# Performance work log

Hardware: AMD Instinct MI355X
Metric: run time of the kernel (lower is better)

Reference implementation:

```python
import jax, jax.numpy as jnp
import numpy as np

B, N, D, H = 4, 2048, 1024, 16
HD = D // H

def setup_inputs() -> dict:
    key = jax.random.key(0)
    ks = jax.random.split(key, 5)
    s = 0.02
    return {
        "x": jax.random.normal(ks[0], (B, N, D), dtype=jnp.float32),
        "W_qkv": jax.random.normal(ks[1], (D, 3 * D), dtype=jnp.float32) * s,
        "b_qkv": jnp.zeros((3 * D,), dtype=jnp.float32),
        "W_proj": jax.random.normal(ks[2], (D, D), dtype=jnp.float32) * s,
        "b_proj": jnp.zeros((D,), dtype=jnp.float32),
    }

def reference(x, W_qkv, b_qkv, W_proj, b_proj):
    scale = HD ** -0.5
    qkv = x @ W_qkv + b_qkv                       # [B,N,3D]
    qkv = qkv.reshape(B, N, 3, H, HD).transpose(2, 0, 3, 1, 4)  # [3,B,H,N,hd]
    q, k, v = qkv[0], qkv[1], qkv[2]
    attn = jnp.einsum('bhqd,bhkd->bhqk', q, k) * scale
    attn = jax.nn.softmax(attn, axis=-1)
    out = jnp.einsum('bhqk,bhkd->bhqd', attn, v)  # [B,H,N,hd]
    out = out.transpose(0, 2, 1, 3).reshape(B, N, D)
    return out @ W_proj + b_proj
```

## Files before the change

kernel.cpp:

```cpp
#include <hip/hip_runtime.h>


typedef __bf16 bf8v  __attribute__((ext_vector_type(8)));
typedef __bf16 bf4v  __attribute__((ext_vector_type(4)));
typedef float  f32x4 __attribute__((ext_vector_type(4)));

typedef const __attribute__((address_space(1))) void* gptr_t;
typedef __attribute__((address_space(3))) void*       lptr_t;

#define GLL16(g, l) __builtin_amdgcn_global_load_lds((gptr_t)(g), (lptr_t)(l), 16, 0, 0)

#define MFMA_BF16_16x16x32 __builtin_amdgcn_mfma_f32_16x16x32_bf16

static constexpr int Bsz = 4, Nseq = 2048, Dmod = 1024, H = 16, HD = 64;
static constexpr int Mtok = Bsz * Nseq;

__global__ __launch_bounds__(256) void cast_f32_bf16(const float* __restrict__ in,
                                                     __bf16* __restrict__ out, int n4) {
    int i = blockIdx.x * blockDim.x + threadIdx.x;
    int stride = gridDim.x * blockDim.x;
    for (; i < n4; i += stride) {
        float4 f = reinterpret_cast<const float4*>(in)[i];
        bf4v o;
        o[0] = (__bf16)f.x; o[1] = (__bf16)f.y; o[2] = (__bf16)f.z; o[3] = (__bf16)f.w;
        reinterpret_cast<bf4v*>(out)[i] = o;
    }
}

__global__ __launch_bounds__(256) void transpose_cast(const float* __restrict__ W,
                                                      __bf16* __restrict__ WT,
                                                      int K, int N) {
    __shared__ float t[32][33];
    int tx = threadIdx.x, ty = threadIdx.y;
    int bx = blockIdx.x, by = blockIdx.y;
#pragma unroll
    for (int j = 0; j < 4; ++j) {
        int k = by * 32 + ty + j * 8;
        int n = bx * 32 + tx;
        t[ty + j * 8][tx] = W[(size_t)k * N + n];
    }
    __syncthreads();
#pragma unroll
    for (int j = 0; j < 4; ++j) {
        int n = bx * 32 + ty + j * 8;
        int k = by * 32 + tx;
        WT[(size_t)n * K + k] = (__bf16)t[tx][ty + j * 8];
    }
}

__global__ __launch_bounds__(256) void transpose_v(const __bf16* __restrict__ V,
                                                   __bf16* __restrict__ VT) {
    __shared__ __bf16 Ls[64 * 72];
    const int t = threadIdx.x;
    const int blk = blockIdx.x;
    const int nt0 = (blk & 31) * 64;
    const size_t base = (size_t)(blk >> 5) * Nseq * HD;
#pragma unroll
    for (int i = 0; i < 2; ++i) {
        int c = i * 256 + t;
        int nt = c >> 3, p = c & 7;
        bf8v v8 = *(const bf8v*)&V[base + (size_t)(nt0 + nt) * HD + p * 8];
#pragma unroll
        for (int j = 0; j < 8; ++j)
            Ls[(p * 8 + j) * 72 + (nt ^ (p << 3))] = v8[j];
    }
    __syncthreads();
#pragma unroll
    for (int i = 0; i < 2; ++i) {
        int c = i * 256 + t;
        int hd = c >> 3, seg = c & 7;
        int key = (hd >> 3) << 3;
        bf8v o = *(const bf8v*)&Ls[hd * 72 + seg * 8];
        int ntb = (seg * 8) ^ (key << 3);
        ntb = (seg * 8) ^ ((hd >> 3) << 3);
        *(bf8v*)&VT[base + (size_t)hd * Nseq + nt0 + ntb] = o;
    }
}

template <int EPI>
__global__ __launch_bounds__(256) void gemm_bt(const __bf16* __restrict__ A,
                                               const __bf16* __restrict__ Bt,
                                               const float* __restrict__ bias,
                                               float* __restrict__ Cf,
                                               __bf16* __restrict__ Qo,
                                               __bf16* __restrict__ Ko,
                                               __bf16* __restrict__ Vo,
                                               int M, int N, int K) {
    __shared__ __attribute__((aligned(16))) __bf16 As[128 * 64];
    __shared__ __attribute__((aligned(16))) __bf16 Bs[128 * 64];

    const int nwg = gridDim.x;
    const int wg = (blockIdx.x & 7) * (nwg >> 3) + (blockIdx.x >> 3);

    const int nbn = N >> 7;
    const int bm = wg / nbn, bn = wg % nbn;
    const int tid = threadIdx.x;
    const int w = tid >> 6, l = tid & 63;
    const int wr = w >> 1, wc = w & 1;

    const int fr = l & 15;
    const int fk = (l >> 4) * 8;

    f32x4 acc[4][4] = {};

    for (int k0 = 0; k0 < K; k0 += 64) {
#pragma unroll
        for (int i = 0; i < 4; ++i) {
            int c = i * 256 + tid;
            int row = c >> 3, col = (c & 7) * 8;
            int scol = col ^ ((row & 7) << 3);
            GLL16(A + (size_t)(bm * 128 + row) * K + k0 + scol, &As[(i * 256 + w * 64) * 8]);
        }
#pragma unroll
        for (int i = 0; i < 4; ++i) {
            int c = i * 256 + tid;
            int row = c >> 3, col = (c & 7) * 8;
            int scol = col ^ ((row & 7) << 3);
            GLL16(Bt + (size_t)(bn * 128 + row) * K + k0 + scol, &Bs[(i * 256 + w * 64) * 8]);
        }
        __syncthreads();

#pragma unroll
        for (int kk = 0; kk < 2; ++kk) {
            bf8v af[4], bf[4];
#pragma unroll
            for (int m = 0; m < 4; ++m) {
                int row = wr * 64 + m * 16 + fr;
                af[m] = *(const bf8v*)&As[row * 64 + ((kk * 32 + fk) ^ ((row & 7) << 3))];
            }
#pragma unroll
            for (int n = 0; n < 4; ++n) {
                int row = wc * 64 + n * 16 + fr;
                bf[n] = *(const bf8v*)&Bs[row * 64 + ((kk * 32 + fk) ^ ((row & 7) << 3))];
            }
#pragma unroll
            for (int m = 0; m < 4; ++m)
#pragma unroll
                for (int n = 0; n < 4; ++n)
                    acc[m][n] = MFMA_BF16_16x16x32(af[m], bf[n], acc[m][n], 0, 0, 0);
        }
        __syncthreads();
    }

    const int r0 = bm * 128 + wr * 64;
    const int c0 = bn * 128 + wc * 64;
#pragma unroll
    for (int m = 0; m < 4; ++m)
#pragma unroll
        for (int n = 0; n < 4; ++n)
#pragma unroll
            for (int r = 0; r < 4; ++r) {
                int row = r0 + m * 16 + (l >> 4) * 4 + r;
                int col = c0 + n * 16 + (l & 15);
                float v = acc[m][n][r] + bias[col];
                if (EPI == 0) {
                    int mat = col >> 10, rem = col & 1023;
                    int h = rem >> 6, hd = rem & 63;
                    int b = row >> 11, nt = row & 2047;
                    size_t dst = (((size_t)(b * H + h)) * Nseq + nt) * HD + hd;
                    __bf16 val = (__bf16)v;
                    if (mat == 0)      Qo[dst] = val;
                    else if (mat == 1) Ko[dst] = val;
                    else               Vo[dst] = val;
                } else {
                    Cf[(size_t)row * N + col] = v;
                }
            }
}

__global__ __launch_bounds__(256, 3) void attn_kernel(const __bf16* __restrict__ Q,
                                                      const __bf16* __restrict__ K,
                                                      const __bf16* __restrict__ VT,
                                                      __bf16* __restrict__ Ao) {
    __shared__ __attribute__((aligned(16))) __bf16 Ks[2][64 * 64];
    __shared__ __attribute__((aligned(16))) __bf16 Vts[2][64 * 64];
    __shared__ __attribute__((aligned(16))) __bf16 Pl[4][32 * 72];

    const int tid = threadIdx.x;
    const int w = tid >> 6, l = tid & 63;

    const int nwg = gridDim.x;
    const int id = (blockIdx.x & 7) * (nwg >> 3) + (blockIdx.x >> 3);
    const int qb = id & 15;
    const int h = (id >> 4) & 15;
    const int b = id >> 8;
    const size_t base = (size_t)(b * H + h) * Nseq * HD;

    const int fr = l & 15;
    const int fkh = (l >> 4) * 8;

    const int sr0 = tid >> 3, sp0 = tid & 7;
    const int sr1 = (256 + tid) >> 3, sp1 = tid & 7;

    bf8v qf[2][2];
#pragma unroll
    for (int m = 0; m < 2; ++m) {
        const int qrow = qb * 128 + w * 32 + m * 16 + fr;
        qf[m][0] = *(const bf8v*)&Q[base + (size_t)qrow * HD + fkh];
        qf[m][1] = *(const bf8v*)&Q[base + (size_t)qrow * HD + 32 + fkh];
#pragma unroll
        for (int j = 0; j < 8; ++j) {
            qf[m][0][j] = (__bf16)((float)qf[m][0][j] * 0.125f);
            qf[m][1][j] = (__bf16)((float)qf[m][1][j] * 0.125f);
        }
    }

    f32x4 o[2][4] = {};
    f32x4 psum[2] = {};

#define STAGE(buf, kt)                                                                   \
    do {                                                                                 \
        GLL16(K  + base + (size_t)((kt) * 64 + sr0) * HD + ((sp0 ^ (sr0 & 7)) << 3),     \
              &Ks[buf][(w * 64) * 8]);                                                   \
        GLL16(K  + base + (size_t)((kt) * 64 + sr1) * HD + ((sp1 ^ (sr1 & 7)) << 3),     \
              &Ks[buf][(256 + w * 64) * 8]);                                             \
        GLL16(VT + base + (size_t)sr0 * Nseq + (kt) * 64 + ((sp0 ^ (sr0 & 7)) << 3),     \
              &Vts[buf][(w * 64) * 8]);                                                  \
        GLL16(VT + base + (size_t)sr1 * Nseq + (kt) * 64 + ((sp1 ^ (sr1 & 7)) << 3),     \
              &Vts[buf][(256 + w * 64) * 8]);                                            \
    } while (0)

    STAGE(0, 0);

    for (int kt = 0; kt < Nseq / 64; ++kt) {
        const int cur = kt & 1;
        if (kt < Nseq / 64 - 1) {
            STAGE(cur ^ 1, kt + 1);
            asm volatile("s_waitcnt vmcnt(4)" ::: "memory");
        } else {
            asm volatile("s_waitcnt vmcnt(0)" ::: "memory");
        }
        __builtin_amdgcn_s_barrier();

        f32x4 s[2][4];
        __builtin_amdgcn_s_setprio(1);
#pragma unroll
        for (int st = 0; st < 4; ++st) {
            const int krow = st * 16 + fr;
            const int key = (fr & 7) << 3;
            bf8v kf0 = *(const bf8v*)&Ks[cur][krow * 64 + (fkh ^ key)];
            bf8v kf1 = *(const bf8v*)&Ks[cur][krow * 64 + ((fkh + 32) ^ key)];
#pragma unroll
            for (int m = 0; m < 2; ++m) {
                f32x4 a = {};
                a = MFMA_BF16_16x16x32(qf[m][0], kf0, a, 0, 0, 0);
                a = MFMA_BF16_16x16x32(qf[m][1], kf1, a, 0, 0, 0);
                s[m][st] = a;
            }
        }
        __builtin_amdgcn_s_setprio(0);

#pragma unroll
        for (int m = 0; m < 2; ++m)
#pragma unroll
            for (int st = 0; st < 4; ++st)
#pragma unroll
                for (int r = 0; r < 4; ++r) {
                    float p = __expf(s[m][st][r]);
                    psum[m][r] += p;
                    const int qr = m * 16 + (l >> 4) * 4 + r;
                    Pl[w][qr * 72 + st * 16 + (l & 15)] = (__bf16)p;
                }

        bf8v pa[2][2];
#pragma unroll
        for (int m = 0; m < 2; ++m) {
            const int prow = m * 16 + fr;
            pa[m][0] = *(const bf8v*)&Pl[w][prow * 72 + fkh];
            pa[m][1] = *(const bf8v*)&Pl[w][prow * 72 + 32 + fkh];
        }
        __builtin_amdgcn_s_setprio(1);
#pragma unroll
        for (int t = 0; t < 4; ++t) {
            const int drow = t * 16 + fr;
            const int key = (fr & 7) << 3;
            bf8v vf0 = *(const bf8v*)&Vts[cur][drow * 64 + (fkh ^ key)];
            bf8v vf1 = *(const bf8v*)&Vts[cur][drow * 64 + ((fkh + 32) ^ key)];
#pragma unroll
            for (int m = 0; m < 2; ++m) {
                o[m][t] = MFMA_BF16_16x16x32(pa[m][0], vf0, o[m][t], 0, 0, 0);
                o[m][t] = MFMA_BF16_16x16x32(pa[m][1], vf1, o[m][t], 0, 0, 0);
            }
        }
        __builtin_amdgcn_s_setprio(0);
        __builtin_amdgcn_s_barrier();
    }
#undef STAGE

#pragma unroll
    for (int m = 0; m < 2; ++m)
#pragma unroll
        for (int r = 0; r < 4; ++r) {
            float ps = psum[m][r];
#pragma unroll
            for (int off = 1; off < 16; off <<= 1) ps += __shfl_xor(ps, off);
            psum[m][r] = 1.f / ps;
        }
#pragma unroll
    for (int m = 0; m < 2; ++m)
#pragma unroll
        for (int t = 0; t < 4; ++t)
#pragma unroll
            for (int r = 0; r < 4; ++r) {
                const int row = m * 16 + (l >> 4) * 4 + r;
                const int nq = qb * 128 + w * 32 + row;
                const int hd = t * 16 + (l & 15);
                Ao[((size_t)(b * Nseq + nq)) * Dmod + h * HD + hd] =
                    (__bf16)(o[m][t][r] * psum[m][r]);
            }
}

extern "C" void kernel_launch(void* const* d_in, const int* in_sizes, int n_in,
                              void* d_out, int out_size, void* d_ws, size_t ws_size,
                              hipStream_t stream) {
    const float* x      = (const float*)d_in[0];
    const float* W_qkv  = (const float*)d_in[1];
    const float* b_qkv  = (const float*)d_in[2];
    const float* W_proj = (const float*)d_in[3];
    const float* b_proj = (const float*)d_in[4];
    float* out = (float*)d_out;

    char* ws = (char*)d_ws;
    __bf16* Xb     = (__bf16*)(ws);
    __bf16* VTb    = (__bf16*)(ws);
    __bf16* WqkvT  = (__bf16*)(ws + 16777216);
    __bf16* WprojT = (__bf16*)(ws + 23068672);
    __bf16* Qb     = (__bf16*)(ws + 25165824);
    __bf16* Kb     = (__bf16*)(ws + 41943040);
    __bf16* Vb     = (__bf16*)(ws + 58720256);
    __bf16* Ab     = (__bf16*)(ws + 58720256);

    cast_f32_bf16<<<2048, 256, 0, stream>>>(x, Xb, Mtok * Dmod / 4);

    dim3 tb(32, 8);
    transpose_cast<<<dim3(3 * Dmod / 32, Dmod / 32), tb, 0, stream>>>(W_qkv, WqkvT, Dmod, 3 * Dmod);
    transpose_cast<<<dim3(Dmod / 32, Dmod / 32), tb, 0, stream>>>(W_proj, WprojT, Dmod, Dmod);

    gemm_bt<0><<<(Mtok / 128) * (3 * Dmod / 128), 256, 0, stream>>>(
        Xb, WqkvT, b_qkv, nullptr, Qb, Kb, Vb, Mtok, 3 * Dmod, Dmod);

    transpose_v<<<Bsz * H * (Nseq / 64), 256, 0, stream>>>(Vb, VTb);

    attn_kernel<<<Bsz * H * (Nseq / 128), 256, 0, stream>>>(Qb, Kb, VTb, Ab);

    gemm_bt<1><<<(Mtok / 128) * (Dmod / 128), 256, 0, stream>>>(
        Ab, WprojT, b_proj, out, nullptr, nullptr, nullptr, Mtok, Dmod, Dmod);
}
```

Before: 299.8 us.

## Switch attention to 32x32 MFMA with register-resident P via permlane swap

Rewrites the attention inner loop to use 32x32x16 MFMAs with S computed transposed (K as A operand), so the exponentiated probabilities stay in registers. The P tile is repacked with v_cvt_pk_bf16_f32 and v_permlane32_swap into the A-operand layout for the PV MFMA, which removes the per-wave LDS round trip for P and the Pl shared buffer. Row sums reduce with one cross-half shuffle, and the epilogue is rewritten for the 32x32 output layout. This cuts LDS traffic and LDS capacity, but it depends on getting the lane-mapping transpose exactly right, and the output stores are now strided per row.

```diff
diff --git a/kernel.cpp b/kernel.cpp
--- a/kernel.cpp
+++ b/kernel.cpp
@@ -1,9 +1,10 @@
 #include <hip/hip_runtime.h>
 
 
-typedef __bf16 bf8v  __attribute__((ext_vector_type(8)));
-typedef __bf16 bf4v  __attribute__((ext_vector_type(4)));
-typedef float  f32x4 __attribute__((ext_vector_type(4)));
+typedef __bf16 bf8v   __attribute__((ext_vector_type(8)));
+typedef __bf16 bf4v   __attribute__((ext_vector_type(4)));
+typedef float  f32x4  __attribute__((ext_vector_type(4)));
+typedef float  f32x16 __attribute__((ext_vector_type(16)));
 
 typedef const __attribute__((address_space(1))) void* gptr_t;
 typedef __attribute__((address_space(3))) void*       lptr_t;
@@ -11,6 +12,7 @@
 #define GLL16(g, l) __builtin_amdgcn_global_load_lds((gptr_t)(g), (lptr_t)(l), 16, 0, 0)
 
 #define MFMA_BF16_16x16x32 __builtin_amdgcn_mfma_f32_16x16x32_bf16
+#define MFMA_BF16_32x32x16 __builtin_amdgcn_mfma_f32_32x32x16_bf16
 
 static constexpr int Bsz = 4, Nseq = 2048, Dmod = 1024, H = 16, HD = 64;
 static constexpr int Mtok = Bsz * Nseq;
@@ -69,10 +71,8 @@
     for (int i = 0; i < 2; ++i) {
         int c = i * 256 + t;
         int hd = c >> 3, seg = c & 7;
-        int key = (hd >> 3) << 3;
         bf8v o = *(const bf8v*)&Ls[hd * 72 + seg * 8];
-        int ntb = (seg * 8) ^ (key << 3);
-        ntb = (seg * 8) ^ ((hd >> 3) << 3);
+        int ntb = (seg * 8) ^ ((hd >> 3) << 3);
         *(bf8v*)&VT[base + (size_t)hd * Nseq + nt0 + ntb] = o;
     }
 }
@@ -174,10 +174,11 @@
                                                       __bf16* __restrict__ Ao) {
     __shared__ __attribute__((aligned(16))) __bf16 Ks[2][64 * 64];
     __shared__ __attribute__((aligned(16))) __bf16 Vts[2][64 * 64];
-    __shared__ __attribute__((aligned(16))) __bf16 Pl[4][32 * 72];
 
     const int tid = threadIdx.x;
     const int w = tid >> 6, l = tid & 63;
+    const int lq = l & 31;
+    const int hi = l >> 5;
 
     const int nwg = gridDim.x;
     const int id = (blockIdx.x & 7) * (nwg >> 3) + (blockIdx.x >> 3);
@@ -186,27 +187,21 @@
     const int b = id >> 8;
     const size_t base = (size_t)(b * H + h) * Nseq * HD;
 
-    const int fr = l & 15;
-    const int fkh = (l >> 4) * 8;
-
     const int sr0 = tid >> 3, sp0 = tid & 7;
     const int sr1 = (256 + tid) >> 3, sp1 = tid & 7;
 
-    bf8v qf[2][2];
-#pragma unroll
-    for (int m = 0; m < 2; ++m) {
-        const int qrow = qb * 128 + w * 32 + m * 16 + fr;
-        qf[m][0] = *(const bf8v*)&Q[base + (size_t)qrow * HD + fkh];
-        qf[m][1] = *(const bf8v*)&Q[base + (size_t)qrow * HD + 32 + fkh];
-#pragma unroll
-        for (int j = 0; j < 8; ++j) {
-            qf[m][0][j] = (__bf16)((float)qf[m][0][j] * 0.125f);
-            qf[m][1][j] = (__bf16)((float)qf[m][1][j] * 0.125f);
-        }
-    }
-
-    f32x4 o[2][4] = {};
-    f32x4 psum[2] = {};
+    const int qrow = qb * 128 + w * 32 + lq;
+    bf8v qf[4];
+#pragma unroll
+    for (int c = 0; c < 4; ++c) {
+        qf[c] = *(const bf8v*)&Q[base + (size_t)qrow * HD + c * 16 + hi * 8];
+#pragma unroll
+        for (int j = 0; j < 8; ++j)
+            qf[c][j] = (__bf16)((float)qf[c][j] * 0.125f);
+    }
+
+    f32x16 o[2] = {};
+    float psum = 0.f;
 
 #define STAGE(buf, kt)                                                                   \
     do {                                                                                 \
@@ -232,82 +227,75 @@
         }
         __builtin_amdgcn_s_barrier();
 
-        f32x4 s[2][4];
+        f32x16 s[2];
         __builtin_amdgcn_s_setprio(1);
 #pragma unroll
-        for (int st = 0; st < 4; ++st) {
-            const int krow = st * 16 + fr;
-            const int key = (fr & 7) << 3;
-            bf8v kf0 = *(const bf8v*)&Ks[cur][krow * 64 + (fkh ^ key)];
-            bf8v kf1 = *(const bf8v*)&Ks[cur][krow * 64 + ((fkh + 32) ^ key)];
-#pragma unroll
-            for (int m = 0; m < 2; ++m) {
-                f32x4 a = {};
-                a = MFMA_BF16_16x16x32(qf[m][0], kf0, a, 0, 0, 0);
-                a = MFMA_BF16_16x16x32(qf[m][1], kf1, a, 0, 0, 0);
-                s[m][st] = a;
-            }
+        for (int sub = 0; sub < 2; ++sub) {
+            const int krow = sub * 32 + lq;
+            const int key = (lq & 7) << 3;
+            f32x16 a = {};
+#pragma unroll
+            for (int c = 0; c < 4; ++c) {
+                bf8v kf = *(const bf8v*)&Ks[cur][krow * 64 + ((c * 16 + hi * 8) ^ key)];
+                a = MFMA_BF16_32x32x16(kf, qf[c], a, 0, 0, 0);
+            }
+            s[sub] = a;
         }
         __builtin_amdgcn_s_setprio(0);
 
 #pragma unroll
-        for (int m = 0; m < 2; ++m)
-#pragma unroll
-            for (int st = 0; st < 4; ++st)
-#pragma unroll
-                for (int r = 0; r < 4; ++r) {
-                    float p = __expf(s[m][st][r]);
-                    psum[m][r] += p;
-                    const int qr = m * 16 + (l >> 4) * 4 + r;
-                    Pl[w][qr * 72 + st * 16 + (l & 15)] = (__bf16)p;
+        for (int sub = 0; sub < 2; ++sub) {
+            int W[4][2];
+#pragma unroll
+            for (int g = 0; g < 4; ++g)
+#pragma unroll
+                for (int wp = 0; wp < 2; ++wp) {
+                    float e0 = __expf(s[sub][g * 4 + wp * 2]);
+                    float e1 = __expf(s[sub][g * 4 + wp * 2 + 1]);
+                    psum += e0 + e1;
+                    int pk;
+                    asm("v_cvt_pk_bf16_f32 %0, %1, %2" : "=v"(pk) : "v"(e0), "v"(e1));
+                    W[g][wp] = pk;
                 }
-
-        bf8v pa[2][2];
-#pragma unroll
-        for (int m = 0; m < 2; ++m) {
-            const int prow = m * 16 + fr;
-            pa[m][0] = *(const bf8v*)&Pl[w][prow * 72 + fkh];
-            pa[m][1] = *(const bf8v*)&Pl[w][prow * 72 + 32 + fkh];
-        }
-        __builtin_amdgcn_s_setprio(1);
-#pragma unroll
-        for (int t = 0; t < 4; ++t) {
-            const int drow = t * 16 + fr;
-            const int key = (fr & 7) << 3;
-            bf8v vf0 = *(const bf8v*)&Vts[cur][drow * 64 + (fkh ^ key)];
-            bf8v vf1 = *(const bf8v*)&Vts[cur][drow * 64 + ((fkh + 32) ^ key)];
-#pragma unroll
-            for (int m = 0; m < 2; ++m) {
-                o[m][t] = MFMA_BF16_16x16x32(pa[m][0], vf0, o[m][t], 0, 0, 0);
-                o[m][t] = MFMA_BF16_16x16x32(pa[m][1], vf1, o[m][t], 0, 0, 0);
-            }
-        }
-        __builtin_amdgcn_s_setprio(0);
+#pragma unroll
+            for (int cp = 0; cp < 2; ++cp) {
+                int x0 = W[2 * cp][0], y0 = W[2 * cp + 1][0];
+                int x1 = W[2 * cp][1], y1 = W[2 * cp + 1][1];
+                asm volatile("v_permlane32_swap_b32 %0, %1" : "+v"(x0), "+v"(y0));
+                asm volatile("v_permlane32_swap_b32 %0, %1" : "+v"(x1), "+v"(y1));
+                union { int wrd[4]; bf8v v; } fu;
+                fu.wrd[0] = x0; fu.wrd[1] = x1; fu.wrd[2] = y0; fu.wrd[3] = y1;
+                const bf8v pa = fu.v;
+
+                const int cg = sub * 2 + cp;
+                __builtin_amdgcn_s_setprio(1);
+#pragma unroll
+                for (int n = 0; n < 2; ++n) {
+                    const int drow = n * 32 + lq;
+                    bf8v vf = *(const bf8v*)&Vts[cur][drow * 64 +
+                                                      ((cg * 16 + hi * 8) ^ ((lq & 7) << 3))];
+                    o[n] = MFMA_BF16_32x32x16(pa, vf, o[n], 0, 0, 0);
+                }
+                __builtin_amdgcn_s_setprio(0);
+            }
+        }
         __builtin_amdgcn_s_barrier();
     }
 #undef STAGE
 
-#pragma unroll
-    for (int m = 0; m < 2; ++m)
-#pragma unroll
-        for (int r = 0; r < 4; ++r) {
-            float ps = psum[m][r];
-#pragma unroll
-            for (int off = 1; off < 16; off <<= 1) ps += __shfl_xor(ps, off);
-            psum[m][r] = 1.f / ps;
-        }
-#pragma unroll
-    for (int m = 0; m < 2; ++m)
-#pragma unroll
-        for (int t = 0; t < 4; ++t)
-#pragma unroll
-            for (int r = 0; r < 4; ++r) {
-                const int row = m * 16 + (l >> 4) * 4 + r;
-                const int nq = qb * 128 + w * 32 + row;
-                const int hd = t * 16 + (l & 15);
-                Ao[((size_t)(b * Nseq + nq)) * Dmod + h * HD + hd] =
-                    (__bf16)(o[m][t][r] * psum[m][r]);
-            }
+    psum += __shfl_xor(psum, 32);
+    const float inv = 1.f / psum;
+
+#pragma unroll
+    for (int r = 0; r < 16; ++r) {
+        const int qr = (r & 3) + 8 * (r >> 2);
+        const float iv = __shfl(inv, qr + 4 * hi);
+        const int nq = qb * 128 + w * 32 + qr + 4 * hi;
+        const size_t rowbase = ((size_t)(b * Nseq + nq)) * Dmod + h * HD;
+#pragma unroll
+        for (int n = 0; n < 2; ++n)
+            Ao[rowbase + n * 32 + lq] = (__bf16)(o[n][r] * iv);
+    }
 }
 
 extern "C" void kernel_launch(void* const* d_in, const int* in_sizes, int n_in,
```

New measurement: 280.8 us. 6.3% less time.
